# Performance work log

Measured on AMD Instinct MI355X. Metric: run time of the kernel, lower is better.

Reference implementation:

```python
import jax, jax.numpy as jnp
import numpy as np

T, B, I, H, C, O = 4096, 8, 256, 512, 1024, 512
SCHEDULE = 1.0
UPPER_T = 0.3
NIND = int((1.0 - SCHEDULE) * (C - 2) * UPPER_T) + 1  # = 1 (argmax WTA)


def setup_inputs() -> dict:
    key = jax.random.key(0)
    ks = jax.random.split(key, 8)
    def lin(k, fan_out, fan_in):
        s = 1.0 / np.sqrt(fan_in)
        kw, kb = jax.random.split(k)
        return (jax.random.uniform(kw, (fan_out, fan_in), jnp.float32, -s, s),
                jax.random.uniform(kb, (fan_out,), jnp.float32, -s, s))
    i2m_w, i2m_b = lin(ks[0], H, I)
    m2h_w, m2h_b = lin(ks[1], C, H)
    h2o_w, h2o_b = lin(ks[2], O, C)
    return {
        "x": jax.random.normal(ks[3], (T, B, I), jnp.float32),
        "hidden1": jnp.zeros((1,), jnp.float32),  # unused dummy (overwritten in torch forward)
        "i2m_w": i2m_w, "i2m_b": i2m_b,
        "m2h_w": m2h_w, "m2h_b": m2h_b,
        "h2o_w": h2o_w, "h2o_b": h2o_b,
    }


def reference(x, hidden1, i2m_w, i2m_b, m2h_w, m2h_b, h2o_w, h2o_b):
    # linear -> relu
    h = jax.nn.relu(jnp.einsum('tbi,hi->tbh', x, i2m_w) + i2m_b)
    # linear -> relu -> concept pre-activations [T,B,C]
    c = jax.nn.relu(jnp.einsum('tbh,ch->tbc', h, m2h_w) + m2h_b)
    # winner-take-all: top-Nind scatter mask (replaces CPU argsort round-trip)
    _, idx = jax.lax.top_k(c, NIND)  # [T,B,NIND]
    t_ix = jnp.arange(c.shape[0])[:, None, None]
    b_ix = jnp.arange(c.shape[1])[None, :, None]
    mask = jnp.zeros_like(c).at[t_ix, b_ix, idx].set(1.0)
    m = c * mask
    # L2 normalize over concept axis
    m = m / jnp.linalg.norm(m, axis=-1, keepdims=True)
    out = jnp.einsum('tbc,oc->tbo', m, h2o_w) + h2o_b
    return jax.nn.log_softmax(out, axis=-1)
```

## Files before the change

### kernel.cpp

```cpp
#include <hip/hip_runtime.h>
#include <stdint.h>

#define M_ROWS 32768
#define I_DIM 256
#define H_DIM 512
#define C_DIM 1024
#define O_DIM 512

typedef __attribute__((ext_vector_type(8))) short bf16x8;
typedef __attribute__((ext_vector_type(4))) float f32x4;

__device__ __forceinline__ ushort bf16_rne(float f) {
    unsigned u = __float_as_uint(f);
    unsigned r = u + 0x7FFFu + ((u >> 16) & 1u);
    return (ushort)(r >> 16);
}
__device__ __forceinline__ float bf16_f32(ushort h) {
    return __uint_as_float(((unsigned)h) << 16);
}
__device__ __forceinline__ void split2(float f, ushort& hi, ushort& mid) {
    hi = bf16_rne(f);
    mid = bf16_rne(f - bf16_f32(hi));
}

__device__ __forceinline__ void async_ld16(const void* g, void* l) {
    __builtin_amdgcn_global_load_lds(
        (const __attribute__((address_space(1))) void*)g,
        (__attribute__((address_space(3))) void*)l, 16, 0, 0);
}

__device__ __forceinline__ unsigned long long packvi(float v, int col) {
    unsigned u = __float_as_uint(v);
    u = (u & 0x80000000u) ? ~u : (u | 0x80000000u);
    return ((unsigned long long)u << 32) | (unsigned)(~col);
}

__device__ __forceinline__ int slot_of(int kc, int row) {
    return (kc + ((row >> 1) & 3)) & 3;
}

__global__ __launch_bounds__(256)
void prep(const float* __restrict__ W1, ushort* __restrict__ w1h, ushort* __restrict__ w1m,
          const float* __restrict__ W2, ushort* __restrict__ w2h, ushort* __restrict__ w2m,
          const float* __restrict__ Wo, const float* __restrict__ bo,
          float* __restrict__ LS, unsigned long long* __restrict__ part) {
    __shared__ float sred[4];
    const int b = blockIdx.x;
    const int t = threadIdx.x;
    if (b < 320) {
        const int isW1 = (b < 64);
        const float* W = isW1 ? W1 : W2;
        ushort* hh = isW1 ? w1h : w2h;
        ushort* mm = isW1 ? w1m : w2m;
        const int K = isW1 ? I_DIM : H_DIM;
        const int cpr = K >> 3;
        int gid = (isW1 ? b : b - 64) * 256 + t;
        int row = gid / cpr;
        int rem = gid - row * cpr;
        int g = rem >> 2, kc = rem & 3;
        float4 v0 = *(const float4*)(W + (size_t)gid * 8);
        float4 v1 = *(const float4*)(W + (size_t)gid * 8 + 4);
        __align__(16) ushort h[8], m[8];
        float f[8];
        *(float4*)&f[0] = v0; *(float4*)&f[4] = v1;
        #pragma unroll
        for (int j = 0; j < 8; ++j) split2(f[j], h[j], m[j]);
        size_t dst = (size_t)row * K + g * 32 + slot_of(kc, row) * 8;
        *(uint4*)(hh + dst) = *(uint4*)h;
        *(uint4*)(mm + dst) = *(uint4*)m;
    } else if (b < 1344) {
        const int j = b - 320;
        float l0 = Wo[(size_t)t * C_DIM + j] + bo[t];
        float l1 = Wo[(size_t)(t + 256) * C_DIM + j] + bo[t + 256];

        float mx = fmaxf(l0, l1);
        #pragma unroll
        for (int off = 1; off < 64; off <<= 1)
            mx = fmaxf(mx, __shfl_xor(mx, off, 64));
        if ((t & 63) == 0) sred[t >> 6] = mx;
        __syncthreads();
        mx = fmaxf(fmaxf(sred[0], sred[1]), fmaxf(sred[2], sred[3]));
        __syncthreads();

        float s = expf(l0 - mx) + expf(l1 - mx);
        #pragma unroll
        for (int off = 1; off < 64; off <<= 1)
            s += __shfl_xor(s, off, 64);
        if ((t & 63) == 0) sred[t >> 6] = s;
        __syncthreads();
        s = sred[0] + sred[1] + sred[2] + sred[3];

        float lse = mx + logf(s);
        LS[(size_t)j * O_DIM + t] = l0 - lse;
        LS[(size_t)j * O_DIM + t + 256] = l1 - lse;
    } else {
        part[(b - 1344) * 256 + t] = 0ull;
    }
}

__global__ __launch_bounds__(512, 2)
void gemm1_mfma(const float* __restrict__ X, const ushort* __restrict__ W1h,
                const ushort* __restrict__ W1m, const float* __restrict__ b1,
                ushort* __restrict__ Hh, ushort* __restrict__ Hm) {
    __shared__ __align__(16) ushort SMEM[65536];

    const int tid = threadIdx.x;
    const int lane = tid & 63, wave = tid >> 6;
    const int wm = wave >> 2, wn = wave & 3;
    const int lcol = lane & 15, quad = lane >> 4;
    const int lrow = lane >> 2, lk = (lane & 3) * 8;

    const int d = blockIdx.x;
    const int q = d >> 3;
    const int mT = ((d & 7) << 4) + (q >> 1);
    const int nT = q & 1;
    const int mBase = mT * 256;
    const int nBase = nT * 256;

    const int s_row = tid >> 1, s_half = tid & 1;
    const int sl0 = slot_of(s_half * 2,     s_row);
    const int sl1 = slot_of(s_half * 2 + 1, s_row);
    const float* xrow = X + (size_t)(mBase + s_row) * I_DIM + s_half * 16;

    const int bplane = wave >> 2;
    const int brow0 = (wave & 3) * 64;
    const ushort* wp = bplane ? W1m : W1h;
    const ushort* gks = wp + (size_t)(nBase + brow0 + lrow) * I_DIM + lk;

    f32x4 acc[8][4];
    #pragma unroll
    for (int i = 0; i < 8; ++i)
        #pragma unroll
        for (int j = 0; j < 4; ++j)
            acc[i][j] = (f32x4){0.f, 0.f, 0.f, 0.f};

    int aoff[8], boff[4];
    #pragma unroll
    for (int t = 0; t < 8; ++t) {
        int ra = wm * 128 + t * 16 + lcol;
        aoff[t] = ra * 32 + slot_of(quad, ra) * 8;
    }
    #pragma unroll
    for (int t = 0; t < 4; ++t) {
        int rb = wn * 64 + t * 16 + lcol;
        boff[t] = rb * 32 + slot_of(quad, rb) * 8;
    }

    auto loadX = [&](float* f, int k0) {
        const float* ap = xrow + k0;
        *(float4*)&f[0]  = ((const float4*)ap)[0];
        *(float4*)&f[4]  = ((const float4*)ap)[1];
        *(float4*)&f[8]  = ((const float4*)ap)[2];
        *(float4*)&f[12] = ((const float4*)ap)[3];
    };
    auto stageB = [&](int buf, int k0) {
        ushort* bb = SMEM + 32768 + buf * 16384 + bplane * 8192 + brow0 * 32;
        #pragma unroll
        for (int j = 0; j < 4; ++j)
            async_ld16(gks + k0 + (size_t)(j * 16) * I_DIM, bb + j * 512);
    };
    auto writeA = [&](int buf, const float* f) {
        ushort* a0 = SMEM + buf * 16384;
        ushort* a1 = a0 + 8192;
        bf16x8 h0, h1, m0, m1;
        #pragma unroll
        for (int j = 0; j < 8; ++j) {
            ushort hu, mu;
            split2(f[j], hu, mu);
            h0[j] = (short)hu; m0[j] = (short)mu;
            split2(f[j + 8], hu, mu);
            h1[j] = (short)hu; m1[j] = (short)mu;
        }
        *(bf16x8*)&a0[s_row * 32 + sl0 * 8] = h0;
        *(bf16x8*)&a0[s_row * 32 + sl1 * 8] = h1;
        *(bf16x8*)&a1[s_row * 32 + sl0 * 8] = m0;
        *(bf16x8*)&a1[s_row * 32 + sl1 * 8] = m1;
    };

    {
        float fx[16];
        loadX(fx, 0);
        stageB(0, 0);
        writeA(0, fx);
    }
    asm volatile("s_waitcnt lgkmcnt(0)" ::: "memory");
    asm volatile("s_waitcnt vmcnt(0)" ::: "memory");
    __builtin_amdgcn_s_barrier();
    __builtin_amdgcn_sched_barrier(0);

    const int NK = I_DIM / 32;
    #pragma unroll 2
    for (int ks = 0; ks < NK; ++ks) {
        const int cur = ks & 1;
        const bool more = (ks + 1 < NK);
        const ushort* Ac0 = SMEM + cur * 16384;
        const ushort* Ac1 = Ac0 + 8192;
        const ushort* Bc0 = SMEM + 32768 + cur * 16384;
        const ushort* Bc1 = Bc0 + 8192;

        float fn[16];
        if (more) {
            loadX(fn, (ks + 1) * 32);
            stageB(cur ^ 1, (ks + 1) * 32);
            __builtin_amdgcn_sched_barrier(0);
        }

        bf16x8 bh[4], bm[4];
        #pragma unroll
        for (int nt = 0; nt < 4; ++nt) {
            bh[nt] = *(const bf16x8*)&Bc0[boff[nt]];
            bm[nt] = *(const bf16x8*)&Bc1[boff[nt]];
        }
        #pragma unroll
        for (int half = 0; half < 2; ++half) {
            bf16x8 ah[4], am[4];
            #pragma unroll
            for (int mt = 0; mt < 4; ++mt) {
                ah[mt] = *(const bf16x8*)&Ac0[aoff[half * 4 + mt]];
                am[mt] = *(const bf16x8*)&Ac1[aoff[half * 4 + mt]];
            }
            __builtin_amdgcn_s_setprio(1);
            #pragma unroll
            for (int nt = 0; nt < 4; ++nt) {
                #pragma unroll
                for (int mt = 0; mt < 4; ++mt) {
                    f32x4 a = acc[half * 4 + mt][nt];
                    a = __builtin_amdgcn_mfma_f32_16x16x32_bf16(am[mt], bh[nt], a, 0, 0, 0);
                    a = __builtin_amdgcn_mfma_f32_16x16x32_bf16(ah[mt], bm[nt], a, 0, 0, 0);
                    a = __builtin_amdgcn_mfma_f32_16x16x32_bf16(ah[mt], bh[nt], a, 0, 0, 0);
                    acc[half * 4 + mt][nt] = a;
                }
            }
            __builtin_amdgcn_s_setprio(0);
        }

        if (more) writeA(cur ^ 1, fn);
        asm volatile("s_waitcnt lgkmcnt(0)" ::: "memory");
        if (more)
            asm volatile("s_waitcnt vmcnt(0)" ::: "memory");
        __builtin_amdgcn_s_barrier();
        __builtin_amdgcn_sched_barrier(0);
    }

    #pragma unroll
    for (int plane = 0; plane < 2; ++plane) {
        __syncthreads();
        #pragma unroll
        for (int nt = 0; nt < 4; ++nt) {
            int colRel = wn * 64 + nt * 16 + lcol;
            int g = colRel >> 5, kc = (colRel >> 3) & 3, pos = colRel & 7;
            float bias = b1[nBase + colRel];
            #pragma unroll
            for (int mt = 0; mt < 8; ++mt) {
                #pragma unroll
                for (int r = 0; r < 4; ++r) {
                    int rowRel = wm * 128 + mt * 16 + quad * 4 + r;
                    float v = fmaxf(acc[mt][nt][r] + bias, 0.f);
                    ushort hu, mu;
                    split2(v, hu, mu);
                    SMEM[rowRel * 256 + g * 32 + slot_of(kc, rowRel) * 8 + pos]
                        = plane ? mu : hu;
                }
            }
        }
        __syncthreads();
        ushort* dstp = plane ? Hm : Hh;
        #pragma unroll
        for (int l2 = 0; l2 < 16; ++l2) {
            int c = l2 * 512 + tid;
            int row = c >> 5, idx = c & 31;
            *(uint4*)(dstp + (size_t)(mBase + row) * H_DIM + nBase + idx * 8)
                = *(const uint4*)&SMEM[row * 256 + idx * 8];
        }
    }
}

__global__ __launch_bounds__(512, 2)
void gemm2_mfma(const ushort* __restrict__ Hh, const ushort* __restrict__ Hm,
                const ushort* __restrict__ W2h, const ushort* __restrict__ W2m,
                const float* __restrict__ b2,
                unsigned long long* __restrict__ part) {
    __shared__ __align__(16) ushort As[2][2][8192];
    __shared__ __align__(16) ushort Bs[2][2][8192];
    const int tid = threadIdx.x;
    const int lane = tid & 63, wave = tid >> 6;
    const int wm = wave >> 2, wn = wave & 3;
    const int lcol = lane & 15, quad = lane >> 4;
    const int lrow = lane >> 2, lk = (lane & 3) * 8;

    const int d = blockIdx.x;
    const int l = d >> 3;
    const int mT = ((d & 7) << 4) + (l >> 2);
    const int nT = l & 3;
    const int mBase = mT * 256;
    const int nBase = nT * 256;

    const int m_id = wave >> 1;
    const int shalf = wave & 1;
    const ushort* gsrc;
    ushort* l0;
    ushort* l1;
    switch (m_id) {
        case 0:  gsrc = Hh  + (size_t)mBase * H_DIM; l0 = &As[0][0][0]; l1 = &As[1][0][0]; break;
        case 1:  gsrc = Hm  + (size_t)mBase * H_DIM; l0 = &As[0][1][0]; l1 = &As[1][1][0]; break;
        case 2:  gsrc = W2h + (size_t)nBase * H_DIM; l0 = &Bs[0][0][0]; l1 = &Bs[1][0][0]; break;
        default: gsrc = W2m + (size_t)nBase * H_DIM; l0 = &Bs[0][1][0]; l1 = &Bs[1][1][0]; break;
    }
    l0 += shalf * 4096;
    l1 += shalf * 4096;
    const ushort* gks = gsrc + (size_t)(shalf * 128 + lrow) * H_DIM + lk;

    f32x4 acc[8][4];
    #pragma unroll
    for (int i = 0; i < 8; ++i)
        #pragma unroll
        for (int j = 0; j < 4; ++j)
            acc[i][j] = (f32x4){0.f, 0.f, 0.f, 0.f};

    int aoff[8], boff[4];
    #pragma unroll
    for (int t = 0; t < 8; ++t) {
        int ra = wm * 128 + t * 16 + lcol;
        aoff[t] = ra * 32 + slot_of(quad, ra) * 8;
    }
    #pragma unroll
    for (int t = 0; t < 4; ++t) {
        int rb = wn * 64 + t * 16 + lcol;
        boff[t] = rb * 32 + slot_of(quad, rb) * 8;
    }

    auto stage = [&](ushort* lb, int k0) {
        #pragma unroll
        for (int j = 0; j < 8; ++j)
            async_ld16(gks + k0 + (size_t)(j * 16) * H_DIM, lb + j * 512);
    };

    stage(l0, 0);
    asm volatile("s_waitcnt vmcnt(0)" ::: "memory");
    __builtin_amdgcn_s_barrier();
    __builtin_amdgcn_sched_barrier(0);

    const int NK = H_DIM / 32;
    #pragma unroll 2
    for (int ks = 0; ks < NK; ++ks) {
        const int cur = ks & 1;
        if (ks < NK - 1) {
            stage(cur ? l0 : l1, (ks + 1) * 32);
            __builtin_amdgcn_sched_barrier(0);
        }

        bf16x8 bh[4], bm[4];
        #pragma unroll
        for (int nt = 0; nt < 4; ++nt) {
            bh[nt] = *(const bf16x8*)&Bs[cur][0][boff[nt]];
            bm[nt] = *(const bf16x8*)&Bs[cur][1][boff[nt]];
        }
        #pragma unroll
        for (int half = 0; half < 2; ++half) {
            bf16x8 ah[4], am[4];
            #pragma unroll
            for (int mt = 0; mt < 4; ++mt) {
                ah[mt] = *(const bf16x8*)&As[cur][0][aoff[half * 4 + mt]];
                am[mt] = *(const bf16x8*)&As[cur][1][aoff[half * 4 + mt]];
            }
            __builtin_amdgcn_s_setprio(1);
            #pragma unroll
            for (int nt = 0; nt < 4; ++nt) {
                #pragma unroll
                for (int mt = 0; mt < 4; ++mt) {
                    f32x4 a = acc[half * 4 + mt][nt];
                    a = __builtin_amdgcn_mfma_f32_16x16x32_bf16(am[mt], bh[nt], a, 0, 0, 0);
                    a = __builtin_amdgcn_mfma_f32_16x16x32_bf16(ah[mt], bm[nt], a, 0, 0, 0);
                    a = __builtin_amdgcn_mfma_f32_16x16x32_bf16(ah[mt], bh[nt], a, 0, 0, 0);
                    acc[half * 4 + mt][nt] = a;
                }
            }
            __builtin_amdgcn_s_setprio(0);
        }

        if (ks < NK - 1)
            asm volatile("s_waitcnt vmcnt(0)" ::: "memory");
        __builtin_amdgcn_s_barrier();
        __builtin_amdgcn_sched_barrier(0);
    }

    float bias[4];
    #pragma unroll
    for (int nt = 0; nt < 4; ++nt)
        bias[nt] = b2[nBase + wn * 64 + nt * 16 + lcol];

    #pragma unroll
    for (int mt = 0; mt < 8; ++mt) {
        #pragma unroll
        for (int r = 0; r < 4; ++r) {
            unsigned long long best = 0ull;
            #pragma unroll
            for (int nt = 0; nt < 4; ++nt) {
                int col = nBase + wn * 64 + nt * 16 + lcol;
                float v = acc[mt][nt][r] + bias[nt];
                unsigned long long p = packvi(v, col);
                if (p > best) best = p;
            }
            #pragma unroll
            for (int off = 1; off < 16; off <<= 1) {
                unsigned long long o = __shfl_xor((long long)best, off, 64);
                if (o > best) best = o;
            }
            if (lcol == 0) {
                int row = mBase + wm * 128 + mt * 16 + quad * 4 + r;
                atomicMax(&part[row], best);
            }
        }
    }
}

__global__ __launch_bounds__(256)
void gather_out(const unsigned long long* __restrict__ part,
                const float* __restrict__ LS, float* __restrict__ out) {
    const int tid = threadIdx.x;
    const int row = blockIdx.x * 2 + (tid >> 7);
    const int q = tid & 127;
    unsigned long long best = part[row];
    unsigned u = (unsigned)(best >> 32);
    float v = (u & 0x80000000u) ? __uint_as_float(u ^ 0x80000000u)
                                : __uint_as_float(~u);
    int col = (int)(~(unsigned)best) & (C_DIM - 1);
    int j = (v > 0.f) ? col : 0;
    float4 val = ((const float4*)LS)[(size_t)j * 128 + q];
    ((float4*)out)[(size_t)row * 128 + q] = val;
}

extern "C" void kernel_launch(void* const* d_in, const int* in_sizes, int n_in,
                              void* d_out, int out_size, void* d_ws, size_t ws_size,
                              hipStream_t stream) {
    const float* x     = (const float*)d_in[0];
    const float* i2m_w = (const float*)d_in[2];
    const float* i2m_b = (const float*)d_in[3];
    const float* m2h_w = (const float*)d_in[4];
    const float* m2h_b = (const float*)d_in[5];
    const float* h2o_w = (const float*)d_in[6];
    const float* h2o_b = (const float*)d_in[7];
    float* out = (float*)d_out;

    char* ws = (char*)d_ws;
    ushort* w1h = (ushort*)(ws);
    ushort* w1m = (ushort*)(ws + 262144);
    ushort* w2h = (ushort*)(ws + 524288);
    ushort* w2m = (ushort*)(ws + 1572864);
    float*  LS  = (float*)(ws + 2621440);
    unsigned long long* part = (unsigned long long*)(ws + 4718592);

    ushort* Hh = (ushort*)d_out;
    ushort* Hm = Hh + (size_t)M_ROWS * H_DIM;

    prep<<<1472, 256, 0, stream>>>(i2m_w, w1h, w1m, m2h_w, w2h, w2m,
                                   h2o_w, h2o_b, LS, part);
    gemm1_mfma<<<(M_ROWS / 256) * (H_DIM / 256), 512, 0, stream>>>(
        x, w1h, w1m, i2m_b, Hh, Hm);
    gemm2_mfma<<<(M_ROWS / 256) * (C_DIM / 256), 512, 0, stream>>>(
        Hh, Hm, w2h, w2m, m2h_b, part);
    gather_out<<<M_ROWS / 2, 256, 0, stream>>>(part, LS, out);
}
```

Before: 242.0 us.

## Fuse output gather into gemm2 via per-row-tile last-block counter

Removes the separate gather kernel. Each gemm2 block bumps a per-M-tile atomic counter, and the last of the four N-tile blocks reads the argmax winners and writes that tile's log-softmax rows directly. To make this safe, the H intermediate is re-laid out per M-tile inside the output buffer, so a tile's output rows overwrite only its own H data after all its consumers have finished. This adds a tiny zeroing launch and puts the gather work on the tail blocks of gemm2. The counter reuses workspace that gemm1's weights occupied.

Result: slower. 247.8 us (+2.4%).

```diff
diff --git a/kernel.cpp b/kernel.cpp
--- a/kernel.cpp
+++ b/kernel.cpp
@@ -38,6 +38,9 @@
 __device__ __forceinline__ int slot_of(int kc, int row) {
     return (kc + ((row >> 1) & 3)) & 3;
 }
+
+#define HTILE_STRIDE 262144
+#define HMID_OFF     131072
 
 __global__ __launch_bounds__(256)
 void prep(const float* __restrict__ W1, ushort* __restrict__ w1h, ushort* __restrict__ w1m,
@@ -98,10 +101,15 @@
     }
 }
 
+__global__ __launch_bounds__(128)
+void zero_cnt(unsigned* __restrict__ cnt) {
+    cnt[threadIdx.x] = 0u;
+}
+
 __global__ __launch_bounds__(512, 2)
 void gemm1_mfma(const float* __restrict__ X, const ushort* __restrict__ W1h,
                 const ushort* __restrict__ W1m, const float* __restrict__ b1,
-                ushort* __restrict__ Hh, ushort* __restrict__ Hm) {
+                ushort* __restrict__ Hbase) {
     __shared__ __align__(16) ushort SMEM[65536];
 
     const int tid = threadIdx.x;
@@ -242,6 +250,7 @@
         __builtin_amdgcn_sched_barrier(0);
     }
 
+    ushort* tileH = Hbase + (size_t)mT * HTILE_STRIDE;
     #pragma unroll
     for (int plane = 0; plane < 2; ++plane) {
         __syncthreads();
@@ -264,24 +273,27 @@
             }
         }
         __syncthreads();
-        ushort* dstp = plane ? Hm : Hh;
+        ushort* dstp = tileH + (plane ? HMID_OFF : 0);
         #pragma unroll
         for (int l2 = 0; l2 < 16; ++l2) {
             int c = l2 * 512 + tid;
             int row = c >> 5, idx = c & 31;
-            *(uint4*)(dstp + (size_t)(mBase + row) * H_DIM + nBase + idx * 8)
+            *(uint4*)(dstp + (size_t)row * H_DIM + nBase + idx * 8)
                 = *(const uint4*)&SMEM[row * 256 + idx * 8];
         }
     }
 }
 
 __global__ __launch_bounds__(512, 2)
-void gemm2_mfma(const ushort* __restrict__ Hh, const ushort* __restrict__ Hm,
+void gemm2_mfma(const ushort* __restrict__ Hbase,
                 const ushort* __restrict__ W2h, const ushort* __restrict__ W2m,
                 const float* __restrict__ b2,
-                unsigned long long* __restrict__ part) {
+                unsigned long long* __restrict__ part,
+                unsigned* __restrict__ cnt,
+                const float* __restrict__ LS, float* __restrict__ out) {
     __shared__ __align__(16) ushort As[2][2][8192];
     __shared__ __align__(16) ushort Bs[2][2][8192];
+    __shared__ int last_flag;
     const int tid = threadIdx.x;
     const int lane = tid & 63, wave = tid >> 6;
     const int wm = wave >> 2, wn = wave & 3;
@@ -297,12 +309,13 @@
 
     const int m_id = wave >> 1;
     const int shalf = wave & 1;
+    const ushort* tileH = Hbase + (size_t)mT * HTILE_STRIDE;
     const ushort* gsrc;
     ushort* l0;
     ushort* l1;
     switch (m_id) {
-        case 0:  gsrc = Hh  + (size_t)mBase * H_DIM; l0 = &As[0][0][0]; l1 = &As[1][0][0]; break;
-        case 1:  gsrc = Hm  + (size_t)mBase * H_DIM; l0 = &As[0][1][0]; l1 = &As[1][1][0]; break;
+        case 0:  gsrc = tileH;             l0 = &As[0][0][0]; l1 = &As[1][0][0]; break;
+        case 1:  gsrc = tileH + HMID_OFF;  l0 = &As[0][1][0]; l1 = &As[1][1][0]; break;
         case 2:  gsrc = W2h + (size_t)nBase * H_DIM; l0 = &Bs[0][0][0]; l1 = &Bs[1][0][0]; break;
         default: gsrc = W2m + (size_t)nBase * H_DIM; l0 = &Bs[0][1][0]; l1 = &Bs[1][1][0]; break;
     }
@@ -412,22 +425,34 @@
             }
         }
     }
-}
-
-__global__ __launch_bounds__(256)
-void gather_out(const unsigned long long* __restrict__ part,
-                const float* __restrict__ LS, float* __restrict__ out) {
-    const int tid = threadIdx.x;
-    const int row = blockIdx.x * 2 + (tid >> 7);
-    const int q = tid & 127;
-    unsigned long long best = part[row];
-    unsigned u = (unsigned)(best >> 32);
-    float v = (u & 0x80000000u) ? __uint_as_float(u ^ 0x80000000u)
-                                : __uint_as_float(~u);
-    int col = (int)(~(unsigned)best) & (C_DIM - 1);
-    int j = (v > 0.f) ? col : 0;
-    float4 val = ((const float4*)LS)[(size_t)j * 128 + q];
-    ((float4*)out)[(size_t)row * 128 + q] = val;
+
+    __syncthreads();
+    if (tid == 0) {
+        __threadfence();
+        unsigned old = atomicAdd(cnt + mT, 1u);
+        last_flag = (old == 3u);
+    }
+    __syncthreads();
+    if (last_flag) {
+        int* js = (int*)&As[0][0][0];
+        if (tid < 256) {
+            unsigned long long best = atomicAdd(&part[mBase + tid], 0ull);
+            unsigned u = (unsigned)(best >> 32);
+            float v = (u & 0x80000000u) ? __uint_as_float(u ^ 0x80000000u)
+                                        : __uint_as_float(~u);
+            int col = (int)(~(unsigned)best) & (C_DIM - 1);
+            js[tid] = (v > 0.f) ? col : 0;
+        }
+        __syncthreads();
+        const float4* LS4 = (const float4*)LS;
+        float4* out4 = (float4*)out + (size_t)mBase * 128;
+        #pragma unroll
+        for (int i = 0; i < 64; ++i) {
+            int idx = i * 512 + tid;
+            int row = idx >> 7, q2 = idx & 127;
+            out4[idx] = LS4[(size_t)js[row] * 128 + q2];
+        }
+    }
 }
 
 extern "C" void kernel_launch(void* const* d_in, const int* in_sizes, int n_in,
@@ -449,15 +474,15 @@
     ushort* w2m = (ushort*)(ws + 1572864);
     float*  LS  = (float*)(ws + 2621440);
     unsigned long long* part = (unsigned long long*)(ws + 4718592);
-
-    ushort* Hh = (ushort*)d_out;
-    ushort* Hm = Hh + (size_t)M_ROWS * H_DIM;
+    unsigned* cnt = (unsigned*)(ws);
+
+    ushort* Hbase = (ushort*)d_out;
 
     prep<<<1472, 256, 0, stream>>>(i2m_w, w1h, w1m, m2h_w, w2h, w2m,
                                    h2o_w, h2o_b, LS, part);
     gemm1_mfma<<<(M_ROWS / 256) * (H_DIM / 256), 512, 0, stream>>>(
-        x, w1h, w1m, i2m_b, Hh, Hm);
+        x, w1h, w1m, i2m_b, Hbase);
+    zero_cnt<<<1, 128, 0, stream>>>(cnt);
     gemm2_mfma<<<(M_ROWS / 256) * (C_DIM / 256), 512, 0, stream>>>(
-        Hh, Hm, w2h, w2m, m2h_b, part);
-    gather_out<<<M_ROWS / 2, 256, 0, stream>>>(part, LS, out);
-}
+        Hbase, w2h, w2m, m2h_b, part, cnt, LS, out);
+}
```
